# Optimization experiments

Measured on AMD Instinct MI355X. Metric: run time of the kernel, lower is better.

The kernel has to match this reference:

```python
import jax, jax.numpy as jnp
import numpy as np

N, E, CIN, COUT, KHOP = 100000, 600000, 128, 128, 3


def setup_inputs() -> dict:
    key = jax.random.key(0)
    k1, k2, k3 = jax.random.split(key, 3)
    x = jax.random.normal(k1, (N, CIN), dtype=jnp.float32)
    edge_index = jax.random.randint(k2, (2, E), 0, N, dtype=jnp.int64)
    # xavier_uniform init for weight [in, out]
    limit = float(np.sqrt(6.0 / (CIN + COUT)))
    weight = jax.random.uniform(k3, (CIN, COUT), minval=-limit, maxval=limit, dtype=jnp.float32)
    bias = jnp.zeros((COUT,), jnp.float32)
    log_scale = jnp.asarray(np.log(1.0), jnp.float32)  # init_scale = 1.0
    hop_logits = jnp.zeros((KHOP + 1,), jnp.float32)
    return {"x": x, "edge_index": edge_index, "num_nodes": N,
            "weight": weight, "bias": bias,
            "log_scale": log_scale, "hop_logits": hop_logits}


def reference(x, edge_index, num_nodes, weight, bias, log_scale, hop_logits):
    src, dst = edge_index[0], edge_index[1]
    # symmetric normalization D_src^{-1/2} A D_dst^{-1/2}, no self-loops
    ones = jnp.ones(src.shape, x.dtype)
    deg_src = jax.ops.segment_sum(ones, src, num_segments=num_nodes)
    deg_dst = jax.ops.segment_sum(ones, dst, num_segments=num_nodes)
    dsi = jnp.where(deg_src > 0, jax.lax.rsqrt(jnp.maximum(deg_src, 1.0)), 0.0)
    ddi = jnp.where(deg_dst > 0, jax.lax.rsqrt(jnp.maximum(deg_dst, 1.0)), 0.0)
    edge_weight = dsi[src] * ddi[dst]  # [E]

    s = jnp.exp(log_scale)
    alpha = jax.nn.softmax(hop_logits)  # [k_hop+1]

    wavelet_out = alpha[0] * x
    current = x
    for k in range(1, KHOP + 1):  # small fixed hop count
        # A_hat @ current : gather -> scale -> scatter-add
        current = jax.ops.segment_sum(current[src] * edge_weight[:, None], dst,
                                      num_segments=num_nodes)
        decay = jnp.exp(-s * k)
        wavelet_out = wavelet_out + alpha[k] * decay * current

    return wavelet_out @ weight + bias
```

## Files before the change

kernel.cpp:

```cpp
#include <hip/hip_runtime.h>
#include <hip/hip_bf16.h>

#define C 128

typedef short s16x8 __attribute__((ext_vector_type(8)));
typedef float f32x4 __attribute__((ext_vector_type(4)));

static __device__ __forceinline__ float b2f(unsigned short u) {
    union { unsigned int i; float f; } v;
    v.i = ((unsigned int)u) << 16;
    return v.f;
}
static __device__ __forceinline__ unsigned short f2b(float f) {
    __hip_bfloat16 b = __float2bfloat16(f);
    return *reinterpret_cast<unsigned short*>(&b);
}

__global__ __launch_bounds__(256) void zero_int_kernel(int4* __restrict__ p, long n4) {
    long i = blockIdx.x * 256L + threadIdx.x;
    if (i < n4) p[i] = make_int4(0, 0, 0, 0);
}

__global__ __launch_bounds__(256) void hist_kernel(
    const int* __restrict__ ei, int E,
    int* __restrict__ degs, int* __restrict__ degd) {
    int i = blockIdx.x * 256 + threadIdx.x;
    int e0 = i * 4;
    if (e0 + 4 <= E) {
        int4 s = *(const int4*)(ei + e0);
        int4 d = *(const int4*)(ei + E + e0);
        atomicAdd(&degs[s.x], 1); atomicAdd(&degs[s.y], 1);
        atomicAdd(&degs[s.z], 1); atomicAdd(&degs[s.w], 1);
        atomicAdd(&degd[d.x], 1); atomicAdd(&degd[d.y], 1);
        atomicAdd(&degd[d.z], 1); atomicAdd(&degd[d.w], 1);
    } else {
        for (int e = e0; e < E; ++e) {
            atomicAdd(&degs[ei[e]], 1);
            atomicAdd(&degd[ei[E + e]], 1);
        }
    }
}

__global__ __launch_bounds__(256) void wt_kernel(const float* __restrict__ W,
                                                 unsigned short* __restrict__ WtB,
                                                 const float* __restrict__ log_scale,
                                                 const float* __restrict__ hop_logits,
                                                 float* __restrict__ coef) {
    int tid = blockIdx.x * 256 + threadIdx.x;
    int k = tid & 127, c = tid >> 7;
    WtB[c * 128 + k] = f2b(W[k * 128 + c]);
    if (tid == 0) {
        float s = expf(log_scale[0]);
        float m = hop_logits[0];
        for (int kk = 1; kk < 4; ++kk) m = fmaxf(m, hop_logits[kk]);
        float a[4], sum = 0.0f;
        for (int kk = 0; kk < 4; ++kk) { a[kk] = expf(hop_logits[kk] - m); sum += a[kk]; }
        for (int kk = 0; kk < 4; ++kk) coef[kk] = (a[kk] / sum) * expf(-s * (float)kk);
    }
}

__global__ __launch_bounds__(256) void rpscan_kernel(const int* __restrict__ degd,
                                                     int* __restrict__ rp,
                                                     int* __restrict__ cursor,
                                                     int* __restrict__ gctr, int N) {
    __shared__ int sm[256];
    __shared__ int base_sm;
    int t = threadIdx.x;
    int i = blockIdx.x * 256 + t;
    int v = (i < N) ? degd[i] : 0;
    sm[t] = v;
    __syncthreads();
    for (int off = 1; off < 256; off <<= 1) {
        int add = (t >= off) ? sm[t - off] : 0;
        __syncthreads();
        sm[t] += add;
        __syncthreads();
    }
    if (t == 255) base_sm = atomicAdd(gctr, sm[255]);
    __syncthreads();
    if (i < N) {
        int r = base_sm + sm[t] - v;
        rp[i] = r;
        cursor[i] = r;
    }
}

__global__ __launch_bounds__(256) void scatter_kernel(const int* __restrict__ ei, int E,
                                                      int* __restrict__ cursor,
                                                      const int* __restrict__ degs,
                                                      int2* __restrict__ csr) {
    int i = blockIdx.x * 256 + threadIdx.x;
    int e0 = i * 4;
    if (e0 + 4 <= E) {
        int4 s = *(const int4*)(ei + e0);
        int4 d = *(const int4*)(ei + E + e0);
        float w0 = rsqrtf((float)degs[s.x]);
        float w1 = rsqrtf((float)degs[s.y]);
        float w2 = rsqrtf((float)degs[s.z]);
        float w3 = rsqrtf((float)degs[s.w]);
        int p0 = atomicAdd(&cursor[d.x], 1);
        int p1 = atomicAdd(&cursor[d.y], 1);
        int p2 = atomicAdd(&cursor[d.z], 1);
        int p3 = atomicAdd(&cursor[d.w], 1);
        csr[p0] = make_int2(s.x, __float_as_int(w0));
        csr[p1] = make_int2(s.y, __float_as_int(w1));
        csr[p2] = make_int2(s.z, __float_as_int(w2));
        csr[p3] = make_int2(s.w, __float_as_int(w3));
    } else {
        for (int e = e0; e < E; ++e) {
            int s = ei[e];
            int d = ei[E + e];
            float w = rsqrtf((float)degs[s]);
            int pos = atomicAdd(&cursor[d], 1);
            csr[pos] = make_int2(s, __float_as_int(w));
        }
    }
}

__global__ __launch_bounds__(256) void pull1_kernel(
    const int* __restrict__ rp, const int* __restrict__ degd,
    const int2* __restrict__ csr,
    const float* __restrict__ x, unsigned int* __restrict__ nxt, int N) {
    int wid = (int)((blockIdx.x * 256L + threadIdx.x) >> 6);
    if (wid >= N) return;
    int lane = threadIdx.x & 63;
    int g  = lane >> 5;
    int ls = lane & 31;
    int beg = __builtin_amdgcn_readfirstlane(rp[wid]);
    int cnt = __builtin_amdgcn_readfirstlane(degd[wid]);
    float a0 = 0.f, a1 = 0.f, a2 = 0.f, a3 = 0.f;
    if (cnt > 0) {
        for (int j = 0; j < cnt; j += 8) {
            #pragma unroll
            for (int h = 0; h < 4; ++h) {
                int jj = j + 2 * h + g;
                bool ok = jj < cnt;
                int2 e = csr[beg + (ok ? jj : 0)];
                float w = ok ? __int_as_float(e.y) : 0.0f;
                float4 v = *(const float4*)(x + (long)e.x * C + ls * 4);
                a0 += w * v.x; a1 += w * v.y; a2 += w * v.z; a3 += w * v.w;
            }
        }
        a0 += __shfl_xor(a0, 32, 64);
        a1 += __shfl_xor(a1, 32, 64);
        a2 += __shfl_xor(a2, 32, 64);
        a3 += __shfl_xor(a3, 32, 64);
        float dv = rsqrtf((float)cnt);
        a0 *= dv; a1 *= dv; a2 *= dv; a3 *= dv;
    }
    if (g == 0) {
        uint2 o;
        o.x = (unsigned int)f2b(a0) | ((unsigned int)f2b(a1) << 16);
        o.y = (unsigned int)f2b(a2) | ((unsigned int)f2b(a3) << 16);
        *(uint2*)((unsigned short*)nxt + (long)wid * C + ls * 4) = o;
    }
}

template<int COMBINE>
__global__ __launch_bounds__(256) void pullb_kernel(
    const int* __restrict__ rp, const int* __restrict__ degd,
    const int2* __restrict__ csr,
    const unsigned short* __restrict__ cur,
    unsigned short* __restrict__ nxt,
    const float* __restrict__ x,
    const unsigned short* __restrict__ h1,
    const float* __restrict__ coef, int N) {
    int wid = (int)((blockIdx.x * 256L + threadIdx.x) >> 6);
    if (wid >= N) return;
    int lane = threadIdx.x & 63;
    int g  = lane >> 4;
    int ls = lane & 15;
    int beg = __builtin_amdgcn_readfirstlane(rp[wid]);
    int cnt = __builtin_amdgcn_readfirstlane(degd[wid]);
    float acc[8] = {0.f, 0.f, 0.f, 0.f, 0.f, 0.f, 0.f, 0.f};
    if (cnt > 0) {
        for (int j = 0; j < cnt; j += 8) {
            int2 e0, e1; float w0, w1;
            {
                int jj = j + g;
                bool ok = jj < cnt;
                e0 = csr[beg + (ok ? jj : 0)];
                w0 = ok ? __int_as_float(e0.y) : 0.0f;
            }
            {
                int jj = j + 4 + g;
                bool ok = jj < cnt;
                e1 = csr[beg + (ok ? jj : 0)];
                w1 = ok ? __int_as_float(e1.y) : 0.0f;
            }
            s16x8 u0 = *(const s16x8*)(cur + (long)e0.x * C + ls * 8);
            s16x8 u1 = *(const s16x8*)(cur + (long)e1.x * C + ls * 8);
            #pragma unroll
            for (int k = 0; k < 8; ++k)
                acc[k] += w0 * b2f((unsigned short)u0[k]) + w1 * b2f((unsigned short)u1[k]);
        }
        #pragma unroll
        for (int k = 0; k < 8; ++k) acc[k] += __shfl_xor(acc[k], 16, 64);
        #pragma unroll
        for (int k = 0; k < 8; ++k) acc[k] += __shfl_xor(acc[k], 32, 64);
        float dv = rsqrtf((float)cnt);
        #pragma unroll
        for (int k = 0; k < 8; ++k) acc[k] *= dv;
    }
    if (g == 0) {
        long rb = (long)wid * C + ls * 8;
        float f[8];
        if (COMBINE) {
            float c0 = coef[0], c1 = coef[1], c2 = coef[2], c3 = coef[3];
            float4 xa = *(const float4*)(x + rb);
            float4 xb = *(const float4*)(x + rb + 4);
            s16x8 u1 = *(const s16x8*)(h1 + rb);
            s16x8 u2 = *(const s16x8*)(cur + rb);
            float xv[8] = {xa.x, xa.y, xa.z, xa.w, xb.x, xb.y, xb.z, xb.w};
            #pragma unroll
            for (int k = 0; k < 8; ++k)
                f[k] = c0 * xv[k] + c1 * b2f((unsigned short)u1[k])
                     + c2 * b2f((unsigned short)u2[k]) + c3 * acc[k];
        } else {
            #pragma unroll
            for (int k = 0; k < 8; ++k) f[k] = acc[k];
        }
        uint4 o;
        o.x = (unsigned int)f2b(f[0]) | ((unsigned int)f2b(f[1]) << 16);
        o.y = (unsigned int)f2b(f[2]) | ((unsigned int)f2b(f[3]) << 16);
        o.z = (unsigned int)f2b(f[4]) | ((unsigned int)f2b(f[5]) << 16);
        o.w = (unsigned int)f2b(f[6]) | ((unsigned int)f2b(f[7]) << 16);
        *(uint4*)(nxt + rb) = o;
    }
}

__global__ __launch_bounds__(256) void gemm_kernel(
    const unsigned short* __restrict__ hc,
    const unsigned short* __restrict__ WtB,
    const float* __restrict__ bias,
    float* __restrict__ out, int N) {
    __shared__ unsigned short Wl[128 * 136];
    int t = threadIdx.x;

    #pragma unroll
    for (int i = 0; i < 8; ++i) {
        int ch = t + i * 256;
        int r = ch >> 4;
        int ko = (ch & 15) * 8;
        *(s16x8*)(Wl + r * 136 + ko) = *(const s16x8*)(WtB + r * 128 + ko);
    }
    __syncthreads();

    int wave = t >> 6, lane = t & 63;
    int lsel = lane & 15;
    int lk   = (lane >> 4) * 8;
    int arow = blockIdx.x * 64 + wave * 16 + lsel;
    bool rok = arow < N;
    long rbase = (long)arow * C;

    f32x4 acc[8];
    #pragma unroll
    for (int i = 0; i < 8; ++i) acc[i] = (f32x4){0.f, 0.f, 0.f, 0.f};

    #pragma unroll
    for (int ks = 0; ks < 4; ++ks) {
        int k0 = ks * 32 + lk;
        s16x8 a = rok ? *(const s16x8*)(hc + rbase + k0) : (s16x8)0;
        #pragma unroll
        for (int cf = 0; cf < 8; ++cf) {
            s16x8 b = *(const s16x8*)(Wl + (cf * 16 + lsel) * 136 + k0);
            acc[cf] = __builtin_amdgcn_mfma_f32_16x16x32_bf16(a, b, acc[cf], 0, 0, 0);
        }
    }

    int orow0 = blockIdx.x * 64 + wave * 16 + (lane >> 4) * 4;
    #pragma unroll
    for (int cf = 0; cf < 8; ++cf) {
        int ocol = cf * 16 + lsel;
        float bv = bias[ocol];
        #pragma unroll
        for (int r = 0; r < 4; ++r) {
            int orow = orow0 + r;
            if (orow < N) out[(long)orow * C + ocol] = acc[cf][r] + bv;
        }
    }
}

extern "C" void kernel_launch(void* const* d_in, const int* in_sizes, int n_in,
                              void* d_out, int out_size, void* d_ws, size_t ws_size,
                              hipStream_t stream) {
    const float* x          = (const float*)d_in[0];
    const int*   ei         = (const int*)d_in[1];
    const float* W          = (const float*)d_in[3];
    const float* bias       = (const float*)d_in[4];
    const float* log_scale  = (const float*)d_in[5];
    const float* hop_logits = (const float*)d_in[6];
    float* out = (float*)d_out;

    int N = in_sizes[0] / C;
    int E = in_sizes[1] / 2;

    char* ws = (char*)d_ws;
    size_t hb = (size_t)N * C * sizeof(unsigned short);
    unsigned short* h1 = (unsigned short*)ws;
    unsigned short* h2 = (unsigned short*)(ws + hb);
    unsigned short* hc = (unsigned short*)(ws + 2 * hb);
    int2*  csr     = (int2*)(ws + 3 * hb);
    int*   degs    = (int*)(csr + E);
    int*   degd    = degs + N;
    int*   gctr    = degd + N;
    int*   rp      = gctr + 16;
    int*   cursor  = rp + N;
    float* coef    = (float*)(cursor + N);
    unsigned short* WtB = (unsigned short*)(coef + 4);

    int eb4 = (E / 4 + 255) / 256 + 1;
    int nbk = (N + 255) / 256;
    int pull_blocks = (int)(((long)N * 64 + 255) / 256);

    long zn4 = (2L * N + 16 + 3) / 4;
    zero_int_kernel<<<(int)((zn4 + 255) / 256), 256, 0, stream>>>((int4*)degs, zn4);
    hist_kernel<<<eb4, 256, 0, stream>>>(ei, E, degs, degd);
    wt_kernel<<<64, 256, 0, stream>>>(W, WtB, log_scale, hop_logits, coef);
    rpscan_kernel<<<nbk, 256, 0, stream>>>(degd, rp, cursor, gctr, N);
    scatter_kernel<<<eb4, 256, 0, stream>>>(ei, E, cursor, degs, csr);

    pull1_kernel<<<pull_blocks, 256, 0, stream>>>(rp, degd, csr, x, (unsigned int*)h1, N);
    pullb_kernel<0><<<pull_blocks, 256, 0, stream>>>(rp, degd, csr, h1, h2, x, h1, coef, N);
    pullb_kernel<1><<<pull_blocks, 256, 0, stream>>>(rp, degd, csr, h2, hc, x, h1, coef, N);

    gemm_kernel<<<(N + 63) / 64, 256, 0, stream>>>(hc, WtB, bias, out, N);
}
```

Before: 251.2 us.

## Slice features into channel planes and pack CSR entries into single words

Converts x to bf16 stored as 8 channel-slice planes so each propagation pass gathers from a 16-channel slice per block. The goal is better cache locality for the random neighbour gathers, since each slice plane is small enough to stay resident in L2/LLC. CSR entries shrink from 8 to 4 bytes by packing the source index (20 bits) with a clamped source degree (12 bits), and the rsqrt is recomputed in the pull. In exchange there is an extra conversion pass, narrower 4-byte gathers per lane, and correctness assumptions: N below 2^20 and degree clamping at 4095.

```diff
diff --git a/kernel.cpp b/kernel.cpp
--- a/kernel.cpp
+++ b/kernel.cpp
@@ -14,6 +14,9 @@
 static __device__ __forceinline__ unsigned short f2b(float f) {
     __hip_bfloat16 b = __float2bfloat16(f);
     return *reinterpret_cast<unsigned short*>(&b);
+}
+static __device__ __forceinline__ unsigned int pk2(float a, float b) {
+    return (unsigned int)f2b(a) | ((unsigned int)f2b(b) << 16);
 }
 
 __global__ __launch_bounds__(256) void zero_int_kernel(int4* __restrict__ p, long n4) {
@@ -88,144 +91,100 @@
 __global__ __launch_bounds__(256) void scatter_kernel(const int* __restrict__ ei, int E,
                                                       int* __restrict__ cursor,
                                                       const int* __restrict__ degs,
-                                                      int2* __restrict__ csr) {
+                                                      unsigned int* __restrict__ csrp) {
     int i = blockIdx.x * 256 + threadIdx.x;
     int e0 = i * 4;
     if (e0 + 4 <= E) {
         int4 s = *(const int4*)(ei + e0);
         int4 d = *(const int4*)(ei + E + e0);
-        float w0 = rsqrtf((float)degs[s.x]);
-        float w1 = rsqrtf((float)degs[s.y]);
-        float w2 = rsqrtf((float)degs[s.z]);
-        float w3 = rsqrtf((float)degs[s.w]);
+        unsigned int g0 = (unsigned int)min(degs[s.x], 4095);
+        unsigned int g1 = (unsigned int)min(degs[s.y], 4095);
+        unsigned int g2 = (unsigned int)min(degs[s.z], 4095);
+        unsigned int g3 = (unsigned int)min(degs[s.w], 4095);
         int p0 = atomicAdd(&cursor[d.x], 1);
         int p1 = atomicAdd(&cursor[d.y], 1);
         int p2 = atomicAdd(&cursor[d.z], 1);
         int p3 = atomicAdd(&cursor[d.w], 1);
-        csr[p0] = make_int2(s.x, __float_as_int(w0));
-        csr[p1] = make_int2(s.y, __float_as_int(w1));
-        csr[p2] = make_int2(s.z, __float_as_int(w2));
-        csr[p3] = make_int2(s.w, __float_as_int(w3));
+        csrp[p0] = (g0 << 20) | (unsigned int)s.x;
+        csrp[p1] = (g1 << 20) | (unsigned int)s.y;
+        csrp[p2] = (g2 << 20) | (unsigned int)s.z;
+        csrp[p3] = (g3 << 20) | (unsigned int)s.w;
     } else {
         for (int e = e0; e < E; ++e) {
             int s = ei[e];
             int d = ei[E + e];
-            float w = rsqrtf((float)degs[s]);
+            unsigned int g = (unsigned int)min(degs[s], 4095);
             int pos = atomicAdd(&cursor[d], 1);
-            csr[pos] = make_int2(s, __float_as_int(w));
-        }
-    }
-}
-
-__global__ __launch_bounds__(256) void pull1_kernel(
+            csrp[pos] = (g << 20) | (unsigned int)s;
+        }
+    }
+}
+
+__global__ __launch_bounds__(256) void conv_kernel(const float* __restrict__ x,
+                                                   unsigned int* __restrict__ xs, int N) {
+    int s = blockIdx.y;
+    long i = blockIdx.x * 256L + threadIdx.x;
+    if (i >= (long)N * 8) return;
+    int n = (int)(i >> 3), q = (int)(i & 7);
+    float2 v = *(const float2*)(x + (long)n * C + s * 16 + q * 2);
+    xs[(long)s * N * 8 + i] = pk2(v.x, v.y);
+}
+
+template<int COMBINE>
+__global__ __launch_bounds__(256) void slpull_kernel(
     const int* __restrict__ rp, const int* __restrict__ degd,
-    const int2* __restrict__ csr,
-    const float* __restrict__ x, unsigned int* __restrict__ nxt, int N) {
-    int wid = (int)((blockIdx.x * 256L + threadIdx.x) >> 6);
-    if (wid >= N) return;
-    int lane = threadIdx.x & 63;
-    int g  = lane >> 5;
-    int ls = lane & 31;
-    int beg = __builtin_amdgcn_readfirstlane(rp[wid]);
-    int cnt = __builtin_amdgcn_readfirstlane(degd[wid]);
-    float a0 = 0.f, a1 = 0.f, a2 = 0.f, a3 = 0.f;
+    const unsigned int* __restrict__ csrp,
+    const unsigned int* __restrict__ srcpl,
+    unsigned int* __restrict__ dstpl,
+    const float* __restrict__ x,
+    const unsigned int* __restrict__ s1pl,
+    const float* __restrict__ coef,
+    unsigned int* __restrict__ hc, int N) {
+    int slice = blockIdx.x & 7;
+    int chunk = blockIdx.x >> 3;
+    int t = threadIdx.x;
+    int lane = t & 63;
+    int node = chunk * 32 + (t >> 6) * 8 + (lane >> 3);
+    int q = lane & 7;
+    if (node >= N) return;
+    const unsigned int* sp = srcpl + (long)slice * N * 8;
+    int beg = rp[node];
+    int cnt = degd[node];
+    float ax = 0.f, ay = 0.f;
     if (cnt > 0) {
-        for (int j = 0; j < cnt; j += 8) {
-            #pragma unroll
-            for (int h = 0; h < 4; ++h) {
-                int jj = j + 2 * h + g;
-                bool ok = jj < cnt;
-                int2 e = csr[beg + (ok ? jj : 0)];
-                float w = ok ? __int_as_float(e.y) : 0.0f;
-                float4 v = *(const float4*)(x + (long)e.x * C + ls * 4);
-                a0 += w * v.x; a1 += w * v.y; a2 += w * v.z; a3 += w * v.w;
-            }
-        }
-        a0 += __shfl_xor(a0, 32, 64);
-        a1 += __shfl_xor(a1, 32, 64);
-        a2 += __shfl_xor(a2, 32, 64);
-        a3 += __shfl_xor(a3, 32, 64);
+        int j = 0;
+        for (; j + 2 <= cnt; j += 2) {
+            unsigned int e0 = csrp[beg + j];
+            unsigned int e1 = csrp[beg + j + 1];
+            float w0 = rsqrtf((float)(e0 >> 20));
+            float w1 = rsqrtf((float)(e1 >> 20));
+            unsigned int u0 = sp[(long)(e0 & 0xFFFFFu) * 8 + q];
+            unsigned int u1 = sp[(long)(e1 & 0xFFFFFu) * 8 + q];
+            ax += w0 * b2f((unsigned short)(u0 & 0xffff)) + w1 * b2f((unsigned short)(u1 & 0xffff));
+            ay += w0 * b2f((unsigned short)(u0 >> 16))    + w1 * b2f((unsigned short)(u1 >> 16));
+        }
+        if (j < cnt) {
+            unsigned int e0 = csrp[beg + j];
+            float w0 = rsqrtf((float)(e0 >> 20));
+            unsigned int u0 = sp[(long)(e0 & 0xFFFFFu) * 8 + q];
+            ax += w0 * b2f((unsigned short)(u0 & 0xffff));
+            ay += w0 * b2f((unsigned short)(u0 >> 16));
+        }
         float dv = rsqrtf((float)cnt);
-        a0 *= dv; a1 *= dv; a2 *= dv; a3 *= dv;
-    }
-    if (g == 0) {
-        uint2 o;
-        o.x = (unsigned int)f2b(a0) | ((unsigned int)f2b(a1) << 16);
-        o.y = (unsigned int)f2b(a2) | ((unsigned int)f2b(a3) << 16);
-        *(uint2*)((unsigned short*)nxt + (long)wid * C + ls * 4) = o;
-    }
-}
-
-template<int COMBINE>
-__global__ __launch_bounds__(256) void pullb_kernel(
-    const int* __restrict__ rp, const int* __restrict__ degd,
-    const int2* __restrict__ csr,
-    const unsigned short* __restrict__ cur,
-    unsigned short* __restrict__ nxt,
-    const float* __restrict__ x,
-    const unsigned short* __restrict__ h1,
-    const float* __restrict__ coef, int N) {
-    int wid = (int)((blockIdx.x * 256L + threadIdx.x) >> 6);
-    if (wid >= N) return;
-    int lane = threadIdx.x & 63;
-    int g  = lane >> 4;
-    int ls = lane & 15;
-    int beg = __builtin_amdgcn_readfirstlane(rp[wid]);
-    int cnt = __builtin_amdgcn_readfirstlane(degd[wid]);
-    float acc[8] = {0.f, 0.f, 0.f, 0.f, 0.f, 0.f, 0.f, 0.f};
-    if (cnt > 0) {
-        for (int j = 0; j < cnt; j += 8) {
-            int2 e0, e1; float w0, w1;
-            {
-                int jj = j + g;
-                bool ok = jj < cnt;
-                e0 = csr[beg + (ok ? jj : 0)];
-                w0 = ok ? __int_as_float(e0.y) : 0.0f;
-            }
-            {
-                int jj = j + 4 + g;
-                bool ok = jj < cnt;
-                e1 = csr[beg + (ok ? jj : 0)];
-                w1 = ok ? __int_as_float(e1.y) : 0.0f;
-            }
-            s16x8 u0 = *(const s16x8*)(cur + (long)e0.x * C + ls * 8);
-            s16x8 u1 = *(const s16x8*)(cur + (long)e1.x * C + ls * 8);
-            #pragma unroll
-            for (int k = 0; k < 8; ++k)
-                acc[k] += w0 * b2f((unsigned short)u0[k]) + w1 * b2f((unsigned short)u1[k]);
-        }
-        #pragma unroll
-        for (int k = 0; k < 8; ++k) acc[k] += __shfl_xor(acc[k], 16, 64);
-        #pragma unroll
-        for (int k = 0; k < 8; ++k) acc[k] += __shfl_xor(acc[k], 32, 64);
-        float dv = rsqrtf((float)cnt);
-        #pragma unroll
-        for (int k = 0; k < 8; ++k) acc[k] *= dv;
-    }
-    if (g == 0) {
-        long rb = (long)wid * C + ls * 8;
-        float f[8];
-        if (COMBINE) {
-            float c0 = coef[0], c1 = coef[1], c2 = coef[2], c3 = coef[3];
-            float4 xa = *(const float4*)(x + rb);
-            float4 xb = *(const float4*)(x + rb + 4);
-            s16x8 u1 = *(const s16x8*)(h1 + rb);
-            s16x8 u2 = *(const s16x8*)(cur + rb);
-            float xv[8] = {xa.x, xa.y, xa.z, xa.w, xb.x, xb.y, xb.z, xb.w};
-            #pragma unroll
-            for (int k = 0; k < 8; ++k)
-                f[k] = c0 * xv[k] + c1 * b2f((unsigned short)u1[k])
-                     + c2 * b2f((unsigned short)u2[k]) + c3 * acc[k];
-        } else {
-            #pragma unroll
-            for (int k = 0; k < 8; ++k) f[k] = acc[k];
-        }
-        uint4 o;
-        o.x = (unsigned int)f2b(f[0]) | ((unsigned int)f2b(f[1]) << 16);
-        o.y = (unsigned int)f2b(f[2]) | ((unsigned int)f2b(f[3]) << 16);
-        o.z = (unsigned int)f2b(f[4]) | ((unsigned int)f2b(f[5]) << 16);
-        o.w = (unsigned int)f2b(f[6]) | ((unsigned int)f2b(f[7]) << 16);
-        *(uint4*)(nxt + rb) = o;
+        ax *= dv; ay *= dv;
+    }
+    if (!COMBINE) {
+        dstpl[(long)slice * N * 8 + (long)node * 8 + q] = pk2(ax, ay);
+    } else {
+        float c0 = coef[0], c1 = coef[1], c2 = coef[2], c3 = coef[3];
+        float2 xv = *(const float2*)(x + (long)node * C + slice * 16 + q * 2);
+        unsigned int u1 = s1pl[(long)slice * N * 8 + (long)node * 8 + q];
+        unsigned int u2 = sp[(long)node * 8 + q];
+        float f0 = c0 * xv.x + c1 * b2f((unsigned short)(u1 & 0xffff))
+                 + c2 * b2f((unsigned short)(u2 & 0xffff)) + c3 * ax;
+        float f1 = c0 * xv.y + c1 * b2f((unsigned short)(u1 >> 16))
+                 + c2 * b2f((unsigned short)(u2 >> 16)) + c3 * ay;
+        hc[(long)node * 64 + slice * 8 + q] = pk2(f0, f1);
     }
 }
 
@@ -296,33 +255,36 @@
     int E = in_sizes[1] / 2;
 
     char* ws = (char*)d_ws;
-    size_t hb = (size_t)N * C * sizeof(unsigned short);
-    unsigned short* h1 = (unsigned short*)ws;
-    unsigned short* h2 = (unsigned short*)(ws + hb);
-    unsigned short* hc = (unsigned short*)(ws + 2 * hb);
-    int2*  csr     = (int2*)(ws + 3 * hb);
-    int*   degs    = (int*)(csr + E);
-    int*   degd    = degs + N;
-    int*   gctr    = degd + N;
-    int*   rp      = gctr + 16;
-    int*   cursor  = rp + N;
-    float* coef    = (float*)(cursor + N);
+    size_t plane = (size_t)N * 256;
+    unsigned int* xs = (unsigned int*)ws;
+    unsigned int* s1 = (unsigned int*)(ws + plane);
+    unsigned int* s2 = (unsigned int*)(ws + 2 * plane);
+    unsigned int* csrp = (unsigned int*)(ws + 3 * plane);
+    int*   degs   = (int*)(csrp + E);
+    int*   degd   = degs + N;
+    int*   gctr   = degd + N;
+    int*   rp     = gctr + 16;
+    int*   cursor = rp + N;
+    float* coef   = (float*)(cursor + N);
     unsigned short* WtB = (unsigned short*)(coef + 4);
+    unsigned int* hc = xs;
 
     int eb4 = (E / 4 + 255) / 256 + 1;
     int nbk = (N + 255) / 256;
-    int pull_blocks = (int)(((long)N * 64 + 255) / 256);
+    int slp_blocks = ((N + 31) / 32) * 8;
 
     long zn4 = (2L * N + 16 + 3) / 4;
     zero_int_kernel<<<(int)((zn4 + 255) / 256), 256, 0, stream>>>((int4*)degs, zn4);
     hist_kernel<<<eb4, 256, 0, stream>>>(ei, E, degs, degd);
     wt_kernel<<<64, 256, 0, stream>>>(W, WtB, log_scale, hop_logits, coef);
     rpscan_kernel<<<nbk, 256, 0, stream>>>(degd, rp, cursor, gctr, N);
-    scatter_kernel<<<eb4, 256, 0, stream>>>(ei, E, cursor, degs, csr);
-
-    pull1_kernel<<<pull_blocks, 256, 0, stream>>>(rp, degd, csr, x, (unsigned int*)h1, N);
-    pullb_kernel<0><<<pull_blocks, 256, 0, stream>>>(rp, degd, csr, h1, h2, x, h1, coef, N);
-    pullb_kernel<1><<<pull_blocks, 256, 0, stream>>>(rp, degd, csr, h2, hc, x, h1, coef, N);
-
-    gemm_kernel<<<(N + 63) / 64, 256, 0, stream>>>(hc, WtB, bias, out, N);
-}
+    scatter_kernel<<<eb4, 256, 0, stream>>>(ei, E, cursor, degs, csrp);
+
+    conv_kernel<<<dim3((N * 8 + 255) / 256, 8), 256, 0, stream>>>(x, xs, N);
+
+    slpull_kernel<0><<<slp_blocks, 256, 0, stream>>>(rp, degd, csrp, xs, s1, x, s1, coef, hc, N);
+    slpull_kernel<0><<<slp_blocks, 256, 0, stream>>>(rp, degd, csrp, s1, s2, x, s1, coef, hc, N);
+    slpull_kernel<1><<<slp_blocks, 256, 0, stream>>>(rp, degd, csrp, s2, s2, x, s1, coef, hc, N);
+
+    gemm_kernel<<<(N + 63) / 64, 256, 0, stream>>>((const unsigned short*)hc, WtB, bias, out, N);
+}
```

Result: slower. 345.1 us (+37.4%).

## Store node features and hop intermediates in FP8 for the gather passes

Applied to the files above, without the earlier changes.

Adds a pass that converts x to FP8 (E4M3 via cvt_pk_fp8). All three propagation hops then gather FP8 rows, 128 bytes per node instead of 256 or 512, with one wave per node and each lane owning two channels. This replaces the bf16/fp32 gathers and the cross-lane shuffle reductions. It mainly cuts random-gather memory traffic, but FP8 quantization of x, h1 and h2 adds a lot of numerical error that may break the accuracy tolerance.

```diff
diff --git a/kernel.cpp b/kernel.cpp
--- a/kernel.cpp
+++ b/kernel.cpp
@@ -5,6 +5,7 @@
 
 typedef short s16x8 __attribute__((ext_vector_type(8)));
 typedef float f32x4 __attribute__((ext_vector_type(4)));
+typedef float f32x2 __attribute__((ext_vector_type(2)));
 
 static __device__ __forceinline__ float b2f(unsigned short u) {
     union { unsigned int i; float f; } v;
@@ -117,116 +118,103 @@
     }
 }
 
-__global__ __launch_bounds__(256) void pull1_kernel(
+__global__ __launch_bounds__(256) void conv8_kernel(const float* __restrict__ x,
+                                                    unsigned int* __restrict__ x8, long n4) {
+    long i = blockIdx.x * 256L + threadIdx.x;
+    if (i >= n4) return;
+    float4 v = ((const float4*)x)[i];
+    int r = __builtin_amdgcn_cvt_pk_fp8_f32(v.x, v.y, 0, false);
+    r = __builtin_amdgcn_cvt_pk_fp8_f32(v.z, v.w, r, true);
+    x8[i] = (unsigned int)r;
+}
+
+__global__ __launch_bounds__(256) void pull8_kernel(
     const int* __restrict__ rp, const int* __restrict__ degd,
     const int2* __restrict__ csr,
-    const float* __restrict__ x, unsigned int* __restrict__ nxt, int N) {
+    const unsigned short* __restrict__ src8,
+    unsigned short* __restrict__ dst8, int N) {
     int wid = (int)((blockIdx.x * 256L + threadIdx.x) >> 6);
     if (wid >= N) return;
     int lane = threadIdx.x & 63;
-    int g  = lane >> 5;
-    int ls = lane & 31;
     int beg = __builtin_amdgcn_readfirstlane(rp[wid]);
     int cnt = __builtin_amdgcn_readfirstlane(degd[wid]);
-    float a0 = 0.f, a1 = 0.f, a2 = 0.f, a3 = 0.f;
+    float sx = 0.f, sy = 0.f;
     if (cnt > 0) {
         for (int j = 0; j < cnt; j += 8) {
-            #pragma unroll
-            for (int h = 0; h < 4; ++h) {
-                int jj = j + 2 * h + g;
+            int   idx[8];
+            float wt[8];
+            #pragma unroll
+            for (int i = 0; i < 8; ++i) {
+                int jj = j + i;
                 bool ok = jj < cnt;
                 int2 e = csr[beg + (ok ? jj : 0)];
-                float w = ok ? __int_as_float(e.y) : 0.0f;
-                float4 v = *(const float4*)(x + (long)e.x * C + ls * 4);
-                a0 += w * v.x; a1 += w * v.y; a2 += w * v.z; a3 += w * v.w;
+                idx[i] = e.x;
+                wt[i] = ok ? __int_as_float(e.y) : 0.0f;
             }
-        }
-        a0 += __shfl_xor(a0, 32, 64);
-        a1 += __shfl_xor(a1, 32, 64);
-        a2 += __shfl_xor(a2, 32, 64);
-        a3 += __shfl_xor(a3, 32, 64);
+            unsigned short u[8];
+            #pragma unroll
+            for (int i = 0; i < 8; ++i) u[i] = src8[(long)idx[i] * 64 + lane];
+            #pragma unroll
+            for (int i = 0; i < 8; ++i) {
+                f32x2 v = __builtin_amdgcn_cvt_pk_f32_fp8((int)u[i], false);
+                sx += wt[i] * v[0];
+                sy += wt[i] * v[1];
+            }
+        }
         float dv = rsqrtf((float)cnt);
-        a0 *= dv; a1 *= dv; a2 *= dv; a3 *= dv;
-    }
-    if (g == 0) {
-        uint2 o;
-        o.x = (unsigned int)f2b(a0) | ((unsigned int)f2b(a1) << 16);
-        o.y = (unsigned int)f2b(a2) | ((unsigned int)f2b(a3) << 16);
-        *(uint2*)((unsigned short*)nxt + (long)wid * C + ls * 4) = o;
-    }
-}
-
-template<int COMBINE>
-__global__ __launch_bounds__(256) void pullb_kernel(
+        sx *= dv; sy *= dv;
+    }
+    int pk = __builtin_amdgcn_cvt_pk_fp8_f32(sx, sy, 0, false);
+    dst8[(long)wid * 64 + lane] = (unsigned short)pk;
+}
+
+__global__ __launch_bounds__(256) void pull3c8_kernel(
     const int* __restrict__ rp, const int* __restrict__ degd,
     const int2* __restrict__ csr,
-    const unsigned short* __restrict__ cur,
-    unsigned short* __restrict__ nxt,
+    const unsigned short* __restrict__ h2_8,
     const float* __restrict__ x,
-    const unsigned short* __restrict__ h1,
-    const float* __restrict__ coef, int N) {
+    const unsigned short* __restrict__ h1_8,
+    const float* __restrict__ coef,
+    unsigned int* __restrict__ hc, int N) {
     int wid = (int)((blockIdx.x * 256L + threadIdx.x) >> 6);
     if (wid >= N) return;
     int lane = threadIdx.x & 63;
-    int g  = lane >> 4;
-    int ls = lane & 15;
     int beg = __builtin_amdgcn_readfirstlane(rp[wid]);
     int cnt = __builtin_amdgcn_readfirstlane(degd[wid]);
-    float acc[8] = {0.f, 0.f, 0.f, 0.f, 0.f, 0.f, 0.f, 0.f};
+    float sx = 0.f, sy = 0.f;
     if (cnt > 0) {
         for (int j = 0; j < cnt; j += 8) {
-            int2 e0, e1; float w0, w1;
-            {
-                int jj = j + g;
+            int   idx[8];
+            float wt[8];
+            #pragma unroll
+            for (int i = 0; i < 8; ++i) {
+                int jj = j + i;
                 bool ok = jj < cnt;
-                e0 = csr[beg + (ok ? jj : 0)];
-                w0 = ok ? __int_as_float(e0.y) : 0.0f;
+                int2 e = csr[beg + (ok ? jj : 0)];
+                idx[i] = e.x;
+                wt[i] = ok ? __int_as_float(e.y) : 0.0f;
             }
-            {
-                int jj = j + 4 + g;
-                bool ok = jj < cnt;
-                e1 = csr[beg + (ok ? jj : 0)];
-                w1 = ok ? __int_as_float(e1.y) : 0.0f;
+            unsigned short u[8];
+            #pragma unroll
+            for (int i = 0; i < 8; ++i) u[i] = h2_8[(long)idx[i] * 64 + lane];
+            #pragma unroll
+            for (int i = 0; i < 8; ++i) {
+                f32x2 v = __builtin_amdgcn_cvt_pk_f32_fp8((int)u[i], false);
+                sx += wt[i] * v[0];
+                sy += wt[i] * v[1];
             }
-            s16x8 u0 = *(const s16x8*)(cur + (long)e0.x * C + ls * 8);
-            s16x8 u1 = *(const s16x8*)(cur + (long)e1.x * C + ls * 8);
-            #pragma unroll
-            for (int k = 0; k < 8; ++k)
-                acc[k] += w0 * b2f((unsigned short)u0[k]) + w1 * b2f((unsigned short)u1[k]);
-        }
-        #pragma unroll
-        for (int k = 0; k < 8; ++k) acc[k] += __shfl_xor(acc[k], 16, 64);
-        #pragma unroll
-        for (int k = 0; k < 8; ++k) acc[k] += __shfl_xor(acc[k], 32, 64);
+        }
         float dv = rsqrtf((float)cnt);
-        #pragma unroll
-        for (int k = 0; k < 8; ++k) acc[k] *= dv;
-    }
-    if (g == 0) {
-        long rb = (long)wid * C + ls * 8;
-        float f[8];
-        if (COMBINE) {
-            float c0 = coef[0], c1 = coef[1], c2 = coef[2], c3 = coef[3];
-            float4 xa = *(const float4*)(x + rb);
-            float4 xb = *(const float4*)(x + rb + 4);
-            s16x8 u1 = *(const s16x8*)(h1 + rb);
-            s16x8 u2 = *(const s16x8*)(cur + rb);
-            float xv[8] = {xa.x, xa.y, xa.z, xa.w, xb.x, xb.y, xb.z, xb.w};
-            #pragma unroll
-            for (int k = 0; k < 8; ++k)
-                f[k] = c0 * xv[k] + c1 * b2f((unsigned short)u1[k])
-                     + c2 * b2f((unsigned short)u2[k]) + c3 * acc[k];
-        } else {
-            #pragma unroll
-            for (int k = 0; k < 8; ++k) f[k] = acc[k];
-        }
-        uint4 o;
-        o.x = (unsigned int)f2b(f[0]) | ((unsigned int)f2b(f[1]) << 16);
-        o.y = (unsigned int)f2b(f[2]) | ((unsigned int)f2b(f[3]) << 16);
-        o.z = (unsigned int)f2b(f[4]) | ((unsigned int)f2b(f[5]) << 16);
-        o.w = (unsigned int)f2b(f[6]) | ((unsigned int)f2b(f[7]) << 16);
-        *(uint4*)(nxt + rb) = o;
-    }
+        sx *= dv; sy *= dv;
+    }
+    float c0 = coef[0], c1 = coef[1], c2 = coef[2], c3 = coef[3];
+    long rb = (long)wid * 64 + lane;
+    float2 xv = *(const float2*)(x + (long)wid * C + lane * 2);
+    f32x2 v1 = __builtin_amdgcn_cvt_pk_f32_fp8((int)h1_8[rb], false);
+    f32x2 v2 = __builtin_amdgcn_cvt_pk_f32_fp8((int)h2_8[rb], false);
+    float f0 = c0 * xv.x + c1 * v1[0] + c2 * v2[0] + c3 * sx;
+    float f1 = c0 * xv.y + c1 * v1[1] + c2 * v2[1] + c3 * sy;
+    hc[rb] = (unsigned int)f2b(f0) | ((unsigned int)f2b(f1) << 16);
 }
 
 __global__ __launch_bounds__(256) void gemm_kernel(
@@ -296,11 +284,12 @@
     int E = in_sizes[1] / 2;
 
     char* ws = (char*)d_ws;
-    size_t hb = (size_t)N * C * sizeof(unsigned short);
-    unsigned short* h1 = (unsigned short*)ws;
-    unsigned short* h2 = (unsigned short*)(ws + hb);
-    unsigned short* hc = (unsigned short*)(ws + 2 * hb);
-    int2*  csr     = (int2*)(ws + 3 * hb);
+    size_t f8b = (size_t)N * C;
+    unsigned short* x8  = (unsigned short*)ws;
+    unsigned short* h18 = (unsigned short*)(ws + f8b);
+    unsigned short* h28 = (unsigned short*)(ws + 2 * f8b);
+    unsigned short* hc  = (unsigned short*)(ws + 3 * f8b);
+    int2*  csr     = (int2*)(ws + 5 * f8b);
     int*   degs    = (int*)(csr + E);
     int*   degd    = degs + N;
     int*   gctr    = degd + N;
@@ -320,9 +309,14 @@
     rpscan_kernel<<<nbk, 256, 0, stream>>>(degd, rp, cursor, gctr, N);
     scatter_kernel<<<eb4, 256, 0, stream>>>(ei, E, cursor, degs, csr);
 
-    pull1_kernel<<<pull_blocks, 256, 0, stream>>>(rp, degd, csr, x, (unsigned int*)h1, N);
-    pullb_kernel<0><<<pull_blocks, 256, 0, stream>>>(rp, degd, csr, h1, h2, x, h1, coef, N);
-    pullb_kernel<1><<<pull_blocks, 256, 0, stream>>>(rp, degd, csr, h2, hc, x, h1, coef, N);
+    long n4 = (long)N * C / 4;
+    conv8_kernel<<<(int)((n4 + 255) / 256), 256, 0, stream>>>(x, (unsigned int*)x8, n4);
+
+    pull8_kernel<<<pull_blocks, 256, 0, stream>>>(rp, degd, csr, x8,  h18, N);
+    pull8_kernel<<<pull_blocks, 256, 0, stream>>>(rp, degd, csr, h18, h28, N);
+
+    pull3c8_kernel<<<pull_blocks, 256, 0, stream>>>(rp, degd, csr, h28, x, h18, coef,
+                                                    (unsigned int*)hc, N);
 
     gemm_kernel<<<(N + 63) / 64, 256, 0, stream>>>(hc, WtB, bias, out, N);
 }
```

Result: faster. 233.0 us (-7.2%).
